# Kernel tuning notes

Measured on AMD Instinct MI355X. Metric: run time of the kernel, lower is better.

Reference implementation:

```python
import jax, jax.numpy as jnp
import numpy as np
import math

SHAPES = [(64, 64), (32, 32), (16, 16), (8, 8)]  # (H_l, W_l), sum HW = 5440
N, LQ, D, NH, NL, NP = 4, 5440, 256, 8, 4, 4
HD = D // NH


def _offset_bias():
    thetas = np.arange(NH, dtype=np.float64) * (2.0 * math.pi / NH)
    grid = np.stack([np.cos(thetas), np.sin(thetas)], -1)
    grid = grid / np.abs(grid).max(-1, keepdims=True)
    grid = np.tile(grid[:, None, None, :], (1, NL, NP, 1))
    grid = grid * (np.arange(NP) + 1)[None, None, :, None]
    return jnp.asarray(grid.reshape(-1), jnp.float32)


def setup_inputs() -> dict:
    key = jax.random.key(0)
    ks = jax.random.split(key, 16)
    s = 1.0 / math.sqrt(D)
    inp = {
        'query0': jax.random.normal(ks[0], (N, LQ, D), jnp.float32),
        'query1': jax.random.normal(ks[1], (N, LQ, D), jnp.float32),
        'feat0': jax.random.normal(ks[2], (N, LQ, D), jnp.float32),
        'feat1': jax.random.normal(ks[3], (N, LQ, D), jnp.float32),
        'reference_points': jax.random.uniform(ks[4], (N, LQ, NL, 2), jnp.float32),
        'W_off': 0.01 * jax.random.normal(ks[5], (NH * NL * NP * 2, D), jnp.float32),
        'b_off': _offset_bias(),
        'W_attn': 0.01 * jax.random.normal(ks[6], (NH * NL * NP, D), jnp.float32),
        'b_attn': jnp.zeros((NH * NL * NP,), jnp.float32),
        'W_val': s * jax.random.normal(ks[7], (D, D), jnp.float32),
        'b_val': jnp.zeros((D,), jnp.float32),
        'W_out': s * jax.random.normal(ks[8], (D, D), jnp.float32),
        'b_out': jnp.zeros((D,), jnp.float32),
        'W_agg': s * jax.random.normal(ks[9], (D, 2 * D), jnp.float32),
        'b_agg': jnp.zeros((D,), jnp.float32),
    }
    return inp


def _sample_level(value_l, H, W, loc):
    # value_l: (N, H*W, NH, HD); loc: (N, LQ, NH, NP, 2) normalized in [0,1]
    v_t = value_l.transpose(0, 2, 1, 3)  # (N, NH, HW, HD)
    # grid_sample bilinear, align_corners=False, zero padding:
    x = loc[..., 0] * W - 0.5
    y = loc[..., 1] * H - 0.5
    x0 = jnp.floor(x); y0 = jnp.floor(y)
    lx = x - x0; ly = y - y0
    x0 = x0.astype(jnp.int32); y0 = y0.astype(jnp.int32)

    def corner(xi, yi, w):
        valid = (xi >= 0) & (xi < W) & (yi >= 0) & (yi < H)
        flat = jnp.clip(yi, 0, H - 1) * W + jnp.clip(xi, 0, W - 1)  # (N,LQ,NH,NP)
        ft = flat.transpose(0, 2, 1, 3).reshape(flat.shape[0], flat.shape[2], -1)
        g = jnp.take_along_axis(v_t, ft[..., None], axis=2)  # (N,NH,LQ*NP,HD)
        g = g.reshape(v_t.shape[0], v_t.shape[1], loc.shape[1], loc.shape[3], -1)
        g = g.transpose(0, 2, 1, 3, 4)  # (N,LQ,NH,NP,HD)
        return g * (w * valid)[..., None]

    return (corner(x0, y0, (1 - lx) * (1 - ly)) + corner(x0 + 1, y0, lx * (1 - ly))
            + corner(x0, y0 + 1, (1 - lx) * ly) + corner(x0 + 1, y0 + 1, lx * ly))


def reference(query0, query1, feat0, feat1, reference_points, W_off, b_off,
              W_attn, b_attn, W_val, b_val, W_out, b_out, W_agg, b_agg):
    offset_norm = jnp.asarray([[w, h] for (h, w) in SHAPES], jnp.float32)  # (NL, 2)
    sizes = [h * w for h, w in SHAPES]
    splits = list(np.cumsum(sizes)[:-1])
    outs = []
    for q, feat in ((query0, feat0), (query1, feat1)):
        value = (feat @ W_val.T + b_val).reshape(N, -1, NH, HD)
        off = (q @ W_off.T + b_off).reshape(N, LQ, NH, NL, NP, 2)
        attn = (q @ W_attn.T + b_attn).reshape(N, LQ, NH, NL * NP)
        attn = jax.nn.softmax(attn, axis=-1).reshape(N, LQ, NH, NL, NP)
        loc = reference_points[:, :, None, :, None, :] + off / offset_norm[None, None, None, :, None, :]
        vals = jnp.split(value, splits, axis=1)
        acc = jnp.zeros((N, LQ, NH, HD), value.dtype)
        for l, (H, W) in enumerate(SHAPES):
            s = _sample_level(vals[l], H, W, loc[:, :, :, l])  # (N,LQ,NH,NP,HD)
            acc = acc + jnp.einsum('nqhpd,nqhp->nqhd', s, attn[:, :, :, l])
        outs.append(acc.reshape(N, LQ, D) @ W_out.T + b_out)
    return jnp.concatenate(outs, axis=-1) @ W_agg.T + b_agg
```

## Files before the change

kernel.cpp:

```cpp
#include <hip/hip_runtime.h>
#include <math.h>

#define N_   4
#define LQ_  5440
#define MQ_  (N_*LQ_)

typedef _Float16 f16;
typedef __attribute__((ext_vector_type(2))) _Float16 f16x2;
typedef __attribute__((ext_vector_type(8))) _Float16 f16x8;
typedef __attribute__((ext_vector_type(4))) float     f32x4;

__device__ __forceinline__ unsigned short f2h(float f) {
  union { f16 h; unsigned short u; } v; v.h = (f16)f; return v.u;
}
__device__ __forceinline__ float h2f(unsigned u) {
  union { unsigned short u; f16 h; } v; v.u = (unsigned short)u; return (float)v.h;
}
__device__ __forceinline__ f16x2 u2h2(unsigned u) {
  union { unsigned u; f16x2 h; } v; v.u = u; return v.h;
}

#define GLD16(gp, lp) __builtin_amdgcn_global_load_lds( \
    (const __attribute__((address_space(1))) void*)(gp), \
    (__attribute__((address_space(3))) void*)(lp), 16, 0, 0)

__global__ __launch_bounds__(256)
void prep(const float* __restrict__ W_val, const float* __restrict__ W_off,
          const float* __restrict__ W_attn, const float* __restrict__ W_agg,
          const float* __restrict__ W_out, const float* __restrict__ b_off,
          const float* __restrict__ b_attn, const float* __restrict__ b_agg,
          const float* __restrict__ b_out,
          unsigned short* __restrict__ Wvalh, unsigned short* __restrict__ Wcath,
          unsigned short* __restrict__ Wfinh, float* __restrict__ bcat,
          float* __restrict__ bfin) {
  __shared__ float wrow[256];
  const int b = blockIdx.x, t = threadIdx.x;
  if (b < 160) {
    const float* src; unsigned short* dst; int i;
    if (b < 64)       { src = W_val;  dst = Wvalh;          i = b * 256 + t; }
    else if (b < 128) { src = W_off;  dst = Wcath;          i = (b - 64) * 256 + t; }
    else              { src = W_attn; dst = Wcath + 65536;  i = (b - 128) * 256 + t; }
    float4 v = reinterpret_cast<const float4*>(src)[i];
    ushort4 r;
    r.x = f2h(v.x); r.y = f2h(v.y); r.z = f2h(v.z); r.w = f2h(v.w);
    reinterpret_cast<ushort4*>(dst)[i] = r;
  } else if (b < 672) {
    const int idx = b - 160, j = idx & 255, s = idx >> 8;
    wrow[t] = W_agg[(size_t)j * 512 + s * 256 + t];
    __syncthreads();
    float a = 0.f;
    for (int i = 0; i < 256; ++i) a = fmaf(wrow[i], W_out[(size_t)i * 256 + t], a);
    Wfinh[(size_t)j * 512 + s * 256 + t] = f2h(a);
  } else if (b == 672) {
    float s = b_agg[t];
    for (int i = 0; i < 256; ++i)
      s = fmaf(W_agg[(size_t)t * 512 + i] + W_agg[(size_t)t * 512 + 256 + i], b_out[i], s);
    bfin[t] = s;
  } else if (b == 673) {
    bcat[t] = b_off[t];
  } else {
    if (t < 128) bcat[256 + t] = b_attn[t];
  }
}

__global__ __launch_bounds__(256)
void gemm_stage1(const float* __restrict__ q0, const float* __restrict__ q1,
                 const float* __restrict__ f0, const float* __restrict__ f1,
                 const unsigned short* __restrict__ Wvalh,
                 const unsigned short* __restrict__ Wcath,
                 const float* __restrict__ b_val, const float* __restrict__ bcat,
                 unsigned short* __restrict__ valb, unsigned short* __restrict__ oab) {
  __shared__ __align__(16) unsigned short As[128 * 64];
  __shared__ __align__(16) unsigned short Ws[128 * 64];
  const int y = blockIdx.y, z = blockIdx.z;
  const size_t SZ = (size_t)MQ_ * 256;
  const float* A; const unsigned short* W; const float* bias;
  unsigned short* C; int NC, col0;
  if (y < 2) { A = z ? f1 : f0; W = Wvalh; bias = b_val; C = valb + z * SZ;              NC = 256; col0 = y * 128; }
  else       { A = z ? q1 : q0; W = Wcath; bias = bcat;  C = oab + (size_t)z * MQ_ * 384; NC = 384; col0 = (y - 2) * 128; }

  const int t    = threadIdx.x;
  const int lane = t & 63;
  const int wv   = t >> 6;
  const int wr   = wv >> 1, wc = wv & 1;
  const int row0 = blockIdx.x * 128;
  const int srow = t >> 3, schunk = t & 7;
  const int wbase = wv * 512;

  f32x4 acc[4][4] = {};

  for (int k0 = 0; k0 < 256; k0 += 64) {
    __syncthreads();
    #pragma unroll
    for (int i = 0; i < 4; ++i) {
      const int row = i * 32 + srow;
      const int ch  = schunk ^ (row & 7);
      GLD16(W + (size_t)(col0 + row) * 256 + k0 + ch * 8, &Ws[i * 2048 + wbase]);
    }
    #pragma unroll
    for (int i = 0; i < 4; ++i) {
      const int row = i * 32 + srow;
      const float* src = A + (size_t)(row0 + row) * 256 + k0 + schunk * 8;
      const float4 a0 = *reinterpret_cast<const float4*>(src);
      const float4 a1 = *reinterpret_cast<const float4*>(src + 4);
      f16x8 hv;
      hv[0] = (f16)a0.x; hv[1] = (f16)a0.y; hv[2] = (f16)a0.z; hv[3] = (f16)a0.w;
      hv[4] = (f16)a1.x; hv[5] = (f16)a1.y; hv[6] = (f16)a1.z; hv[7] = (f16)a1.w;
      const int ch = schunk ^ (row & 7);
      *reinterpret_cast<f16x8*>(&As[row * 64 + ch * 8]) = hv;
    }
    __syncthreads();

    f16x8 af[4][2], bfr[4][2];
    #pragma unroll
    for (int f = 0; f < 4; ++f)
      #pragma unroll
      for (int kk = 0; kk < 2; ++kk) {
        const int ra = wr * 64 + f * 16 + (lane & 15);
        const int ca = (kk * 4 + (lane >> 4)) ^ (ra & 7);
        af[f][kk] = *(const f16x8*)&As[ra * 64 + ca * 8];
        const int rb = wc * 64 + f * 16 + (lane & 15);
        const int cb = (kk * 4 + (lane >> 4)) ^ (rb & 7);
        bfr[f][kk] = *(const f16x8*)&Ws[rb * 64 + cb * 8];
      }
    #pragma unroll
    for (int kk = 0; kk < 2; ++kk)
      #pragma unroll
      for (int fm = 0; fm < 4; ++fm)
        #pragma unroll
        for (int fn = 0; fn < 4; ++fn)
          acc[fm][fn] = __builtin_amdgcn_mfma_f32_16x16x32_f16(
              af[fm][kk], bfr[fn][kk], acc[fm][fn], 0, 0, 0);
  }

  #pragma unroll
  for (int fm = 0; fm < 4; ++fm) {
    const int m = row0 + wr * 64 + fm * 16 + (lane >> 4) * 4;
    #pragma unroll
    for (int fn = 0; fn < 4; ++fn) {
      const int c = col0 + wc * 64 + fn * 16 + (lane & 15);
      const float bv = bias[c];
      #pragma unroll
      for (int r = 0; r < 4; ++r)
        C[(size_t)(m + r) * NC + c] = f2h(acc[fm][fn][r] + bv);
    }
  }
}

__global__ __launch_bounds__(256)
void gemm_final(const unsigned short* __restrict__ A,
                const unsigned short* __restrict__ W,
                const float* __restrict__ bias, float* __restrict__ out) {
  __shared__ __align__(16) unsigned short As[128 * 64];
  __shared__ __align__(16) unsigned short Ws[128 * 64];
  const int t    = threadIdx.x;
  const int lane = t & 63;
  const int wv   = t >> 6;
  const int wr   = wv >> 1, wc = wv & 1;
  const int row0 = blockIdx.x * 128, col0 = blockIdx.y * 128;
  const int srow = t >> 3, schunk = t & 7;
  const int wbase = wv * 512;

  f32x4 acc[4][4] = {};

  for (int k0 = 0; k0 < 512; k0 += 64) {
    __syncthreads();
    #pragma unroll
    for (int i = 0; i < 4; ++i) {
      const int row = i * 32 + srow;
      const int ch  = schunk ^ (row & 7);
      GLD16(A + (size_t)(row0 + row) * 512 + k0 + ch * 8, &As[i * 2048 + wbase]);
      GLD16(W + (size_t)(col0 + row) * 512 + k0 + ch * 8, &Ws[i * 2048 + wbase]);
    }
    __syncthreads();

    f16x8 af[4][2], bfr[4][2];
    #pragma unroll
    for (int f = 0; f < 4; ++f)
      #pragma unroll
      for (int kk = 0; kk < 2; ++kk) {
        const int ra = wr * 64 + f * 16 + (lane & 15);
        const int ca = (kk * 4 + (lane >> 4)) ^ (ra & 7);
        af[f][kk] = *(const f16x8*)&As[ra * 64 + ca * 8];
        const int rb = wc * 64 + f * 16 + (lane & 15);
        const int cb = (kk * 4 + (lane >> 4)) ^ (rb & 7);
        bfr[f][kk] = *(const f16x8*)&Ws[rb * 64 + cb * 8];
      }
    #pragma unroll
    for (int kk = 0; kk < 2; ++kk)
      #pragma unroll
      for (int fm = 0; fm < 4; ++fm)
        #pragma unroll
        for (int fn = 0; fn < 4; ++fn)
          acc[fm][fn] = __builtin_amdgcn_mfma_f32_16x16x32_f16(
              af[fm][kk], bfr[fn][kk], acc[fm][fn], 0, 0, 0);
  }

  #pragma unroll
  for (int fm = 0; fm < 4; ++fm) {
    const int m = row0 + wr * 64 + fm * 16 + (lane >> 4) * 4;
    #pragma unroll
    for (int fn = 0; fn < 4; ++fn) {
      const int c = col0 + wc * 64 + fn * 16 + (lane & 15);
      const float bv = bias[c];
      #pragma unroll
      for (int r = 0; r < 4; ++r)
        out[(size_t)(m + r) * 256 + c] = acc[fm][fn][r] + bv;
    }
  }
}

__global__ __launch_bounds__(256, 4)
void deform_sample5(const unsigned short* __restrict__ vals,
                    const unsigned short* __restrict__ oa,
                    const float* __restrict__ refp,
                    unsigned short* __restrict__ acc_out) {
  const int s  = blockIdx.y;
  const int t  = threadIdx.x;
  const int q  = t >> 5, tq = t & 31;
  const int row = blockIdx.x * 8 + q;
  const int n  = row / LQ_;
  const int h  = tq >> 2;
  __shared__ uint4 lds_i[8][16][8];
  __shared__ uint2 lds_w[8][16][8];

  const unsigned short* oar = oa + ((size_t)s * MQ_ + row) * 384;
  {
    const int   l  = tq & 3;
    const int   Wn = 64 >> l;
    const float Wf = (float)Wn;
    const int   lb = (int)(((0xAD200u >> (5 * l)) & 31u) << 8);
    const uint4 ov = *reinterpret_cast<const uint4*>(oar + (size_t)tq * 8);
    const uint2 lv = *reinterpret_cast<const uint2*>(oar + 256 + (size_t)tq * 4);
    const float2 rxy = *reinterpret_cast<const float2*>(refp + (size_t)row * 8 + l * 2);
    float lg[4] = { h2f(lv.x), h2f(lv.x >> 16), h2f(lv.y), h2f(lv.y >> 16) };
    float mx = fmaxf(fmaxf(lg[0], lg[1]), fmaxf(lg[2], lg[3]));
    mx = fmaxf(mx, __shfl_xor(mx, 1));
    mx = fmaxf(mx, __shfl_xor(mx, 2));
    float e[4], se;
    #pragma unroll
    for (int k = 0; k < 4; ++k) e[k] = __expf(lg[k] - mx);
    se = (e[0] + e[1]) + (e[2] + e[3]);
    se += __shfl_xor(se, 1);
    se += __shfl_xor(se, 2);
    const float inv = 1.f / se;
    const unsigned od[4] = { ov.x, ov.y, ov.z, ov.w };
    #pragma unroll
    for (int k = 0; k < 4; ++k) {
      const float ox = h2f(od[k]), oy = h2f(od[k] >> 16);
      const float x = fmaf(rxy.x, Wf, ox) - 0.5f;
      const float y = fmaf(rxy.y, Wf, oy) - 0.5f;
      const float x0f = floorf(x), y0f = floorf(y);
      const int   x0 = (int)x0f,   y0 = (int)y0f;
      const float lx = x - x0f,    ly = y - y0f;
      const float aw = e[k] * inv;
      const int   xs[2] = {x0, x0 + 1}, ys[2] = {y0, y0 + 1};
      const float wx[2] = {1.f - lx, lx}, wy[2] = {1.f - ly, ly};
      unsigned ia[4]; unsigned short wa[4];
      #pragma unroll
      for (int cy = 0; cy < 2; ++cy)
        #pragma unroll
        for (int cx = 0; cx < 2; ++cx) {
          const int xi = xs[cx], yi = ys[cy];
          const bool v = (xi >= 0) && (xi < Wn) && (yi >= 0) && (yi < Wn);
          const int xc = min(max(xi, 0), Wn - 1), yc = min(max(yi, 0), Wn - 1);
          ia[cy * 2 + cx] = (unsigned)(lb + yc * Wn + xc) << 9;
          wa[cy * 2 + cx] = f2h(v ? wx[cx] * wy[cy] * aw : 0.f);
        }
      const int jj = l * 4 + k;
      const int hx = h ^ (jj & 7);
      lds_i[q][jj][hx] = make_uint4(ia[0], ia[1], ia[2], ia[3]);
      lds_w[q][jj][hx] = make_uint2((unsigned)wa[0] | ((unsigned)wa[1] << 16),
                                    (unsigned)wa[2] | ((unsigned)wa[3] << 16));
    }
  }
  __syncthreads();

  const int dg = tq & 3;
  const char* vb = (const char*)(vals + ((size_t)s * N_ + n) * LQ_ * 256);
  const unsigned hd = (unsigned)((h * 32 + dg * 8) * 2);
  float facc[8] = {};
  #pragma unroll 1
  for (int l4 = 0; l4 < 4; ++l4) {
    uint4 mi[4]; uint2 mw[4];
    #pragma unroll
    for (int p = 0; p < 4; ++p) {
      const int j = l4 * 4 + p;
      const int hx = h ^ (j & 7);
      mi[p] = lds_i[q][j][hx];
      mw[p] = lds_w[q][j][hx];
    }
    f16x8 v[16];
    #pragma unroll
    for (int p = 0; p < 4; ++p) {
      v[p * 4 + 0] = *reinterpret_cast<const f16x8*>(vb + (mi[p].x + hd));
      v[p * 4 + 1] = *reinterpret_cast<const f16x8*>(vb + (mi[p].y + hd));
      v[p * 4 + 2] = *reinterpret_cast<const f16x8*>(vb + (mi[p].z + hd));
      v[p * 4 + 3] = *reinterpret_cast<const f16x8*>(vb + (mi[p].w + hd));
    }
    f16x2 a0 = {0, 0}, a1 = {0, 0}, a2 = {0, 0}, a3 = {0, 0};
    #pragma unroll
    for (int p = 0; p < 4; ++p) {
      const f16x2 w0 = u2h2(__builtin_amdgcn_perm(mw[p].x, mw[p].x, 0x01000100u));
      const f16x2 w1 = u2h2(__builtin_amdgcn_perm(mw[p].x, mw[p].x, 0x03020302u));
      const f16x2 w2 = u2h2(__builtin_amdgcn_perm(mw[p].y, mw[p].y, 0x01000100u));
      const f16x2 w3 = u2h2(__builtin_amdgcn_perm(mw[p].y, mw[p].y, 0x03020302u));
      const f16x2* p0 = (const f16x2*)&v[p * 4 + 0];
      const f16x2* p1 = (const f16x2*)&v[p * 4 + 1];
      const f16x2* p2 = (const f16x2*)&v[p * 4 + 2];
      const f16x2* p3 = (const f16x2*)&v[p * 4 + 3];
      a0 = __builtin_elementwise_fma(p0[0], w0, a0);
      a1 = __builtin_elementwise_fma(p0[1], w0, a1);
      a2 = __builtin_elementwise_fma(p0[2], w0, a2);
      a3 = __builtin_elementwise_fma(p0[3], w0, a3);
      a0 = __builtin_elementwise_fma(p1[0], w1, a0);
      a1 = __builtin_elementwise_fma(p1[1], w1, a1);
      a2 = __builtin_elementwise_fma(p1[2], w1, a2);
      a3 = __builtin_elementwise_fma(p1[3], w1, a3);
      a0 = __builtin_elementwise_fma(p2[0], w2, a0);
      a1 = __builtin_elementwise_fma(p2[1], w2, a1);
      a2 = __builtin_elementwise_fma(p2[2], w2, a2);
      a3 = __builtin_elementwise_fma(p2[3], w2, a3);
      a0 = __builtin_elementwise_fma(p3[0], w3, a0);
      a1 = __builtin_elementwise_fma(p3[1], w3, a1);
      a2 = __builtin_elementwise_fma(p3[2], w3, a2);
      a3 = __builtin_elementwise_fma(p3[3], w3, a3);
    }
    facc[0] += (float)a0[0]; facc[1] += (float)a0[1];
    facc[2] += (float)a1[0]; facc[3] += (float)a1[1];
    facc[4] += (float)a2[0]; facc[5] += (float)a2[1];
    facc[6] += (float)a3[0]; facc[7] += (float)a3[1];
  }
  f16x8 r;
  #pragma unroll
  for (int e2 = 0; e2 < 8; ++e2) r[e2] = (f16)facc[e2];
  *reinterpret_cast<f16x8*>(acc_out + (size_t)row * 512 + s * 256 + h * 32 + dg * 8) = r;
}

extern "C" void kernel_launch(void* const* d_in, const int* in_sizes, int n_in,
                              void* d_out, int out_size, void* d_ws, size_t ws_size,
                              hipStream_t stream) {
  const float* query0 = (const float*)d_in[0];
  const float* query1 = (const float*)d_in[1];
  const float* feat0  = (const float*)d_in[2];
  const float* feat1  = (const float*)d_in[3];
  const float* refp   = (const float*)d_in[4];
  const float* W_off  = (const float*)d_in[5];
  const float* b_off  = (const float*)d_in[6];
  const float* W_attn = (const float*)d_in[7];
  const float* b_attn = (const float*)d_in[8];
  const float* W_val  = (const float*)d_in[9];
  const float* b_val  = (const float*)d_in[10];
  const float* W_out  = (const float*)d_in[11];
  const float* b_out  = (const float*)d_in[12];
  const float* W_agg  = (const float*)d_in[13];
  const float* b_agg  = (const float*)d_in[14];
  float* out = (float*)d_out;

  char* p = (char*)d_ws;
  const size_t SZ = (size_t)MQ_ * 256;
  unsigned short* valb  = (unsigned short*)p; p += 2 * SZ * 2;
  unsigned short* oab   = (unsigned short*)p; p += (size_t)2 * MQ_ * 384 * 2;
  unsigned short* accb  = (unsigned short*)p; p += (size_t)MQ_ * 512 * 2;
  unsigned short* Wvalh = (unsigned short*)p; p += 256 * 256 * 2;
  unsigned short* Wcath = (unsigned short*)p; p += 384 * 256 * 2;
  unsigned short* Wfinh = (unsigned short*)p; p += 256 * 512 * 2;
  float* bcat = (float*)p; p += 384 * 4;
  float* bfin = (float*)p; p += 256 * 4;

  prep<<<675, 256, 0, stream>>>(W_val, W_off, W_attn, W_agg, W_out, b_off, b_attn,
                                b_agg, b_out, Wvalh, Wcath, Wfinh, bcat, bfin);
  gemm_stage1<<<dim3(170, 5, 2), 256, 0, stream>>>(query0, query1, feat0, feat1,
                                                   Wvalh, Wcath, b_val, bcat,
                                                   valb, oab);
  deform_sample5<<<dim3(MQ_ / 8, 2), 256, 0, stream>>>(valb, oab, refp, accb);
  gemm_final<<<dim3(170, 2), 256, 0, stream>>>(accb, Wfinh, bfin, out);
}
```

Measured before the change: 161.2 us.

## Loop column tiles inside stage-1 GEMM blocks and pack sampler LDS records

```diff
diff --git a/kernel.cpp b/kernel.cpp
--- a/kernel.cpp
+++ b/kernel.cpp
@@ -72,12 +72,12 @@
                  unsigned short* __restrict__ valb, unsigned short* __restrict__ oab) {
   __shared__ __align__(16) unsigned short As[128 * 64];
   __shared__ __align__(16) unsigned short Ws[128 * 64];
-  const int y = blockIdx.y, z = blockIdx.z;
+  const int src = blockIdx.y, z = blockIdx.z;
   const size_t SZ = (size_t)MQ_ * 256;
   const float* A; const unsigned short* W; const float* bias;
-  unsigned short* C; int NC, col0;
-  if (y < 2) { A = z ? f1 : f0; W = Wvalh; bias = b_val; C = valb + z * SZ;              NC = 256; col0 = y * 128; }
-  else       { A = z ? q1 : q0; W = Wcath; bias = bcat;  C = oab + (size_t)z * MQ_ * 384; NC = 384; col0 = (y - 2) * 128; }
+  unsigned short* C; int NC, NT;
+  if (src == 0) { A = z ? f1 : f0; W = Wvalh; bias = b_val; C = valb + z * SZ;               NC = 256; NT = 2; }
+  else          { A = z ? q1 : q0; W = Wcath; bias = bcat;  C = oab + (size_t)z * MQ_ * 384; NC = 384; NT = 3; }
 
   const int t    = threadIdx.x;
   const int lane = t & 63;
@@ -87,62 +87,65 @@
   const int srow = t >> 3, schunk = t & 7;
   const int wbase = wv * 512;
 
-  f32x4 acc[4][4] = {};
-
-  for (int k0 = 0; k0 < 256; k0 += 64) {
-    __syncthreads();
-    #pragma unroll
-    for (int i = 0; i < 4; ++i) {
-      const int row = i * 32 + srow;
-      const int ch  = schunk ^ (row & 7);
-      GLD16(W + (size_t)(col0 + row) * 256 + k0 + ch * 8, &Ws[i * 2048 + wbase]);
-    }
-    #pragma unroll
-    for (int i = 0; i < 4; ++i) {
-      const int row = i * 32 + srow;
-      const float* src = A + (size_t)(row0 + row) * 256 + k0 + schunk * 8;
-      const float4 a0 = *reinterpret_cast<const float4*>(src);
-      const float4 a1 = *reinterpret_cast<const float4*>(src + 4);
-      f16x8 hv;
-      hv[0] = (f16)a0.x; hv[1] = (f16)a0.y; hv[2] = (f16)a0.z; hv[3] = (f16)a0.w;
-      hv[4] = (f16)a1.x; hv[5] = (f16)a1.y; hv[6] = (f16)a1.z; hv[7] = (f16)a1.w;
-      const int ch = schunk ^ (row & 7);
-      *reinterpret_cast<f16x8*>(&As[row * 64 + ch * 8]) = hv;
-    }
-    __syncthreads();
-
-    f16x8 af[4][2], bfr[4][2];
-    #pragma unroll
-    for (int f = 0; f < 4; ++f)
-      #pragma unroll
-      for (int kk = 0; kk < 2; ++kk) {
-        const int ra = wr * 64 + f * 16 + (lane & 15);
-        const int ca = (kk * 4 + (lane >> 4)) ^ (ra & 7);
-        af[f][kk] = *(const f16x8*)&As[ra * 64 + ca * 8];
-        const int rb = wc * 64 + f * 16 + (lane & 15);
-        const int cb = (kk * 4 + (lane >> 4)) ^ (rb & 7);
-        bfr[f][kk] = *(const f16x8*)&Ws[rb * 64 + cb * 8];
+  for (int ct = 0; ct < NT; ++ct) {
+    const int col0 = ct * 128;
+    f32x4 acc[4][4] = {};
+
+    for (int k0 = 0; k0 < 256; k0 += 64) {
+      __syncthreads();
+      #pragma unroll
+      for (int i = 0; i < 4; ++i) {
+        const int row = i * 32 + srow;
+        const int ch  = schunk ^ (row & 7);
+        GLD16(W + (size_t)(col0 + row) * 256 + k0 + ch * 8, &Ws[i * 2048 + wbase]);
       }
-    #pragma unroll
-    for (int kk = 0; kk < 2; ++kk)
-      #pragma unroll
-      for (int fm = 0; fm < 4; ++fm)
-        #pragma unroll
-        for (int fn = 0; fn < 4; ++fn)
-          acc[fm][fn] = __builtin_amdgcn_mfma_f32_16x16x32_f16(
-              af[fm][kk], bfr[fn][kk], acc[fm][fn], 0, 0, 0);
-  }
-
-  #pragma unroll
-  for (int fm = 0; fm < 4; ++fm) {
-    const int m = row0 + wr * 64 + fm * 16 + (lane >> 4) * 4;
-    #pragma unroll
-    for (int fn = 0; fn < 4; ++fn) {
-      const int c = col0 + wc * 64 + fn * 16 + (lane & 15);
-      const float bv = bias[c];
-      #pragma unroll
-      for (int r = 0; r < 4; ++r)
-        C[(size_t)(m + r) * NC + c] = f2h(acc[fm][fn][r] + bv);
+      #pragma unroll
+      for (int i = 0; i < 4; ++i) {
+        const int row = i * 32 + srow;
+        const float* srcp = A + (size_t)(row0 + row) * 256 + k0 + schunk * 8;
+        const float4 a0 = *reinterpret_cast<const float4*>(srcp);
+        const float4 a1 = *reinterpret_cast<const float4*>(srcp + 4);
+        f16x8 hv;
+        hv[0] = (f16)a0.x; hv[1] = (f16)a0.y; hv[2] = (f16)a0.z; hv[3] = (f16)a0.w;
+        hv[4] = (f16)a1.x; hv[5] = (f16)a1.y; hv[6] = (f16)a1.z; hv[7] = (f16)a1.w;
+        const int ch = schunk ^ (row & 7);
+        *reinterpret_cast<f16x8*>(&As[row * 64 + ch * 8]) = hv;
+      }
+      __syncthreads();
+
+      f16x8 af[4][2], bfr[4][2];
+      #pragma unroll
+      for (int f = 0; f < 4; ++f)
+        #pragma unroll
+        for (int kk = 0; kk < 2; ++kk) {
+          const int ra = wr * 64 + f * 16 + (lane & 15);
+          const int ca = (kk * 4 + (lane >> 4)) ^ (ra & 7);
+          af[f][kk] = *(const f16x8*)&As[ra * 64 + ca * 8];
+          const int rb = wc * 64 + f * 16 + (lane & 15);
+          const int cb = (kk * 4 + (lane >> 4)) ^ (rb & 7);
+          bfr[f][kk] = *(const f16x8*)&Ws[rb * 64 + cb * 8];
+        }
+      #pragma unroll
+      for (int kk = 0; kk < 2; ++kk)
+        #pragma unroll
+        for (int fm = 0; fm < 4; ++fm)
+          #pragma unroll
+          for (int fn = 0; fn < 4; ++fn)
+            acc[fm][fn] = __builtin_amdgcn_mfma_f32_16x16x32_f16(
+                af[fm][kk], bfr[fn][kk], acc[fm][fn], 0, 0, 0);
+    }
+
+    #pragma unroll
+    for (int fm = 0; fm < 4; ++fm) {
+      const int m = row0 + wr * 64 + fm * 16 + (lane >> 4) * 4;
+      #pragma unroll
+      for (int fn = 0; fn < 4; ++fn) {
+        const int c = col0 + wc * 64 + fn * 16 + (lane & 15);
+        const float bv = bias[c];
+        #pragma unroll
+        for (int r = 0; r < 4; ++r)
+          C[(size_t)(m + r) * NC + c] = f2h(acc[fm][fn][r] + bv);
+      }
     }
   }
 }
@@ -211,7 +214,7 @@
 }
 
 __global__ __launch_bounds__(256, 4)
-void deform_sample5(const unsigned short* __restrict__ vals,
+void deform_sample6(const unsigned short* __restrict__ vals,
                     const unsigned short* __restrict__ oa,
                     const float* __restrict__ refp,
                     unsigned short* __restrict__ acc_out) {
@@ -221,8 +224,7 @@
   const int row = blockIdx.x * 8 + q;
   const int n  = row / LQ_;
   const int h  = tq >> 2;
-  __shared__ uint4 lds_i[8][16][8];
-  __shared__ uint2 lds_w[8][16][8];
+  __shared__ uint4 lds_rec[8][16][8];
 
   const unsigned short* oar = oa + ((size_t)s * MQ_ + row) * 384;
   {
@@ -264,14 +266,16 @@
           const int xi = xs[cx], yi = ys[cy];
           const bool v = (xi >= 0) && (xi < Wn) && (yi >= 0) && (yi < Wn);
           const int xc = min(max(xi, 0), Wn - 1), yc = min(max(yi, 0), Wn - 1);
-          ia[cy * 2 + cx] = (unsigned)(lb + yc * Wn + xc) << 9;
+          ia[cy * 2 + cx] = (unsigned)(lb + yc * Wn + xc);
           wa[cy * 2 + cx] = f2h(v ? wx[cx] * wy[cy] * aw : 0.f);
         }
       const int jj = l * 4 + k;
-      const int hx = h ^ (jj & 7);
-      lds_i[q][jj][hx] = make_uint4(ia[0], ia[1], ia[2], ia[3]);
-      lds_w[q][jj][hx] = make_uint2((unsigned)wa[0] | ((unsigned)wa[1] << 16),
-                                    (unsigned)wa[2] | ((unsigned)wa[3] << 16));
+      uint4 rec;
+      rec.x = ia[0] | (ia[1] << 16);
+      rec.y = ia[2] | (ia[3] << 16);
+      rec.z = (unsigned)wa[0] | ((unsigned)wa[1] << 16);
+      rec.w = (unsigned)wa[2] | ((unsigned)wa[3] << 16);
+      lds_rec[q][jj][h ^ (jj & 7)] = rec;
     }
   }
   __syncthreads();
@@ -282,29 +286,27 @@
   float facc[8] = {};
   #pragma unroll 1
   for (int l4 = 0; l4 < 4; ++l4) {
-    uint4 mi[4]; uint2 mw[4];
+    uint4 m[4];
     #pragma unroll
     for (int p = 0; p < 4; ++p) {
       const int j = l4 * 4 + p;
-      const int hx = h ^ (j & 7);
-      mi[p] = lds_i[q][j][hx];
-      mw[p] = lds_w[q][j][hx];
+      m[p] = lds_rec[q][j][h ^ (j & 7)];
     }
     f16x8 v[16];
     #pragma unroll
     for (int p = 0; p < 4; ++p) {
-      v[p * 4 + 0] = *reinterpret_cast<const f16x8*>(vb + (mi[p].x + hd));
-      v[p * 4 + 1] = *reinterpret_cast<const f16x8*>(vb + (mi[p].y + hd));
-      v[p * 4 + 2] = *reinterpret_cast<const f16x8*>(vb + (mi[p].z + hd));
-      v[p * 4 + 3] = *reinterpret_cast<const f16x8*>(vb + (mi[p].w + hd));
+      v[p * 4 + 0] = *reinterpret_cast<const f16x8*>(vb + (((m[p].x & 0xffffu) << 9) + hd));
+      v[p * 4 + 1] = *reinterpret_cast<const f16x8*>(vb + (((m[p].x >> 16) << 9) + hd));
+      v[p * 4 + 2] = *reinterpret_cast<const f16x8*>(vb + (((m[p].y & 0xffffu) << 9) + hd));
+      v[p * 4 + 3] = *reinterpret_cast<const f16x8*>(vb + (((m[p].y >> 16) << 9) + hd));
     }
     f16x2 a0 = {0, 0}, a1 = {0, 0}, a2 = {0, 0}, a3 = {0, 0};
     #pragma unroll
     for (int p = 0; p < 4; ++p) {
-      const f16x2 w0 = u2h2(__builtin_amdgcn_perm(mw[p].x, mw[p].x, 0x01000100u));
-      const f16x2 w1 = u2h2(__builtin_amdgcn_perm(mw[p].x, mw[p].x, 0x03020302u));
-      const f16x2 w2 = u2h2(__builtin_amdgcn_perm(mw[p].y, mw[p].y, 0x01000100u));
-      const f16x2 w3 = u2h2(__builtin_amdgcn_perm(mw[p].y, mw[p].y, 0x03020302u));
+      const f16x2 w0 = u2h2(__builtin_amdgcn_perm(m[p].z, m[p].z, 0x01000100u));
+      const f16x2 w1 = u2h2(__builtin_amdgcn_perm(m[p].z, m[p].z, 0x03020302u));
+      const f16x2 w2 = u2h2(__builtin_amdgcn_perm(m[p].w, m[p].w, 0x01000100u));
+      const f16x2 w3 = u2h2(__builtin_amdgcn_perm(m[p].w, m[p].w, 0x03020302u));
       const f16x2* p0 = (const f16x2*)&v[p * 4 + 0];
       const f16x2* p1 = (const f16x2*)&v[p * 4 + 1];
       const f16x2* p2 = (const f16x2*)&v[p * 4 + 2];
@@ -370,9 +372,9 @@
 
   prep<<<675, 256, 0, stream>>>(W_val, W_off, W_attn, W_agg, W_out, b_off, b_attn,
                                 b_agg, b_out, Wvalh, Wcath, Wfinh, bcat, bfin);
-  gemm_stage1<<<dim3(170, 5, 2), 256, 0, stream>>>(query0, query1, feat0, feat1,
+  gemm_stage1<<<dim3(170, 2, 2), 256, 0, stream>>>(query0, query1, feat0, feat1,
                                                    Wvalh, Wcath, b_val, bcat,
                                                    valb, oab);
-  deform_sample5<<<dim3(MQ_ / 8, 2), 256, 0, stream>>>(valb, oab, refp, accb);
+  deform_sample6<<<dim3(MQ_ / 8, 2), 256, 0, stream>>>(valb, oab, refp, accb);
   gemm_final<<<dim3(170, 2), 256, 0, stream>>>(accb, Wfinh, bfin, out);
 }
```

New measurement: 158.6 us. Within noise of the previous version (-1.6%).
